# Kernel optimization log

Measured on AMD Instinct MI355X. Metric: run time of the kernel, lower is better.

Reference implementation:

```python
import jax, jax.numpy as jnp
import numpy as np

B, N, C, S, K = 2, 2048, 64, 128, 8
RADIUS_PX = 1.5
RAD_POW = 2
TAU = 1.0  # accumulation_tau
RADIUS_NDC = RADIUS_PX / S * 2.0  # radius converted to NDC units, as in forward


def setup_inputs() -> dict:
    key = jax.random.key(0)
    k1, k2, k3 = jax.random.split(key, 3)
    xy = jax.random.uniform(k1, (B, N, 2), minval=-1.0, maxval=1.0)
    z = jax.random.uniform(k2, (B, N, 1), minval=0.1, maxval=5.0)
    pts3D = jnp.concatenate([xy, z], axis=-1)  # [B,N,3] NDC points, z>0
    src = jax.random.normal(k3, (B, C, N), dtype=jnp.float32)  # [B,C,N] features
    return {"pts3D": pts3D, "src": src}


def _rasterize_composite(pts3D, src):
    # sign flip of x,y as in forward (pts3D[:,:,0]=-..., pts3D[:,:,1]=-...)
    pts = pts3D * jnp.array([-1.0, -1.0, 1.0], dtype=pts3D.dtype)
    x, y, z = pts[..., 0], pts[..., 1], pts[..., 2]  # each [B,N]
    # NDC pixel centers (pytorch3d convention: +1 at index 0)
    pix = 1.0 - (2.0 * jnp.arange(S, dtype=pts.dtype) + 1.0) / S  # [S]
    dx2 = (pix[None, :, None] - x[:, None, :]) ** 2  # [B,S_x,N]
    dy2 = (pix[None, :, None] - y[:, None, :]) ** 2  # [B,S_y,N]
    dist2 = dy2[:, :, None, :] + dx2[:, None, :, :]  # [B,S,S,N] squared NDC dist
    in_rad = (dist2 < RADIUS_NDC ** 2) & (z[:, None, None, :] > 0)
    zbuf = jnp.where(in_rad, z[:, None, None, :], jnp.inf)
    # per-pixel z-buffer: K points with smallest z among in-radius points
    negz, idx = jax.lax.top_k(-zbuf, K)  # [B,S,S,K]
    valid = (negz > -jnp.inf).astype(pts.dtype)
    dist_sel = jnp.take_along_axis(dist2, idx, axis=-1)  # [B,S,S,K]
    # dist = dist / radius**rad_pow ; alphas = (1 - clamp(dist,1e-3,1)**0.5)**tau
    dist_n = dist_sel / (RADIUS_NDC ** RAD_POW)
    alphas = (1.0 - jnp.sqrt(jnp.clip(dist_n, 0.001, 1.0))) ** TAU
    alphas = alphas * valid  # empty z-buffer slots contribute nothing
    # gather point features: [B,S,S,K,C]
    feats = src.transpose(0, 2, 1)  # [B,N,C]
    g = jnp.take_along_axis(feats, idx.reshape(B, -1)[..., None], axis=1)
    g = g.reshape(B, S, S, K, C)
    # front-to-back alpha compositing: w_k = a_k * prod_{j<k}(1-a_j)
    trans = jnp.cumprod(1.0 - alphas, axis=-1)
    T = jnp.concatenate([jnp.ones_like(alphas[..., :1]), trans[..., :-1]], axis=-1)
    w = alphas * T  # [B,S,S,K]
    return jnp.einsum('byxk,byxkc->bcyx', w, g)  # [B,C,S,S]


def reference(pts3D, src):
    return _rasterize_composite(pts3D, src)
```

## Files before the change

kernel.cpp:

```cpp
#include <hip/hip_runtime.h>
#include <math.h>

#define NN 2048
#define CC 64
#define SS 128
#define KK 8
#define TCAP 128

#define R2f    0.00054931640625f
#define RNDCf  0.0234375f

__global__ __launch_bounds__(256) void raster_fused_kernel(
    const float* __restrict__ pts3D,
    const float* __restrict__ src,
    float* __restrict__ out)
{
    __shared__ float scx[TCAP];
    __shared__ float scy[TCAP];
    __shared__ unsigned long long skey[TCAP];
    __shared__ int scount;
    __shared__ float sW[KK * 64];
    __shared__ int   sI[KK * 64];

    const int tid = threadIdx.x;
    const int blk = blockIdx.x;
    const int b   = blk >> 8;
    const int tb  = blk & 255;
    const int Y0  = (tb >> 2) * 2;
    const int X0  = (tb & 3) * 32;

    if (tid == 0) scount = 0;
    __syncthreads();

    const float cxmax = 1.0f - (2.0f * (float)X0 + 1.0f) / (float)SS;
    const float cxmin = 1.0f - (2.0f * (float)(X0 + 31) + 1.0f) / (float)SS;
    const float cymax = 1.0f - (2.0f * (float)Y0 + 1.0f) / (float)SS;
    const float cymin = 1.0f - (2.0f * (float)(Y0 + 1) + 1.0f) / (float)SS;
    const float Rm = RNDCf + 1e-6f;

    const float* P = pts3D + (size_t)b * NN * 3;
#pragma unroll
    for (int j = 0; j < NN / 256; ++j) {
        int n = tid + j * 256;
        const float* p = P + (size_t)n * 3;
        float x = -p[0], y = -p[1], z = p[2];
        if (z > 0.0f &&
            x >= cxmin - Rm && x <= cxmax + Rm &&
            y >= cymin - Rm && y <= cymax + Rm) {
            int slot = atomicAdd(&scount, 1);
            if (slot < TCAP) {
                scx[slot] = x;
                scy[slot] = y;
                skey[slot] = ((unsigned long long)__float_as_uint(z) << 32) | (unsigned)n;
            }
        }
    }
    __syncthreads();
    const int cn = min(scount, TCAP);

    if (tid < 64) {
        const int col = tid & 31, r = tid >> 5;
        const int ix = X0 + col, iy = Y0 + r;
        const float pcx = 1.0f - (2.0f * (float)ix + 1.0f) / (float)SS;
        const float pcy = 1.0f - (2.0f * (float)iy + 1.0f) / (float)SS;

        const unsigned long long SENT = ~0ULL;
        unsigned long long s[KK];
        float sd[KK];
#pragma unroll
        for (int j = 0; j < KK; ++j) { s[j] = SENT; sd[j] = 0.0f; }

        for (int i = 0; i < cn; ++i) {
            float dx = pcx - scx[i];
            float dy = pcy - scy[i];
            float d2 = dy * dy + dx * dx;
            unsigned long long k = skey[i];
            if (d2 < R2f && k < s[KK - 1]) {
                float dd = d2;
#pragma unroll
                for (int j = 0; j < KK; ++j) {
                    if (k < s[j]) {
                        unsigned long long tk = s[j]; s[j] = k; k = tk;
                        float td = sd[j]; sd[j] = dd; dd = td;
                    }
                }
            }
        }

        float T = 1.0f;
#pragma unroll
        for (int k = 0; k < KK; ++k) {
            float w = 0.0f; int id = 0;
            if (s[k] != SENT) {
                id = (int)(unsigned)(s[k] & 0xffffffffu);
                float dn = sd[k] / R2f;
                dn = fminf(fmaxf(dn, 0.001f), 1.0f);
                float a = 1.0f - sqrtf(dn);
                w = a * T;
                T *= (1.0f - a);
            }
            sW[k * 64 + tid] = w;
            sI[k * 64 + tid] = id;
        }
    }
    __syncthreads();

    const int px = tid & 63;
    const int cg = tid >> 6;
    float w[KK]; int id[KK];
#pragma unroll
    for (int k = 0; k < KK; ++k) {
        w[k]  = sW[k * 64 + px];
        id[k] = sI[k * 64 + px];
    }
    const int col = px & 31, r = px >> 5;
    float* O = out + (size_t)b * CC * (SS * SS) + (size_t)(Y0 + r) * SS + (X0 + col);
    const float* F = src + (size_t)b * CC * NN;
#pragma unroll 4
    for (int cc = 0; cc < CC / 4; ++cc) {
        int c = cg * (CC / 4) + cc;
        const float* Fc = F + (size_t)c * NN;
        float acc = 0.0f;
#pragma unroll
        for (int k = 0; k < KK; ++k) acc += w[k] * Fc[id[k]];
        O[(size_t)c * (SS * SS)] = acc;
    }
}

extern "C" void kernel_launch(void* const* d_in, const int* in_sizes, int n_in,
                              void* d_out, int out_size, void* d_ws, size_t ws_size,
                              hipStream_t stream) {
    const float* pts3D = (const float*)d_in[0];
    const float* src   = (const float*)d_in[1];
    float* out = (float*)d_out;
    (void)in_sizes; (void)n_in; (void)out_size; (void)d_ws; (void)ws_size;

    raster_fused_kernel<<<dim3(512), dim3(256), 0, stream>>>(pts3D, src, out);
}
```

Baseline: 73.95 us.

## Pre-sort candidates by depth and split channels across twice as many blocks

Candidate points for each tile are now rank-sorted by (z, index) key in shared memory. Each pixel thread then takes the first K in-radius points in that order, which replaces the per-pixel insertion sort over K registers. The grid doubles: each tile is processed by two blocks that each write half of the channels. The launch-bounds occupancy hint is raised as well. The cost is that point culling and the sort run twice per tile, plus an O(cn^2) rank computation in shared memory.

```diff
diff --git a/kernel.cpp b/kernel.cpp
--- a/kernel.cpp
+++ b/kernel.cpp
@@ -10,26 +10,29 @@
 #define R2f    0.00054931640625f
 #define RNDCf  0.0234375f
 
-__global__ __launch_bounds__(256) void raster_fused_kernel(
+__global__ __launch_bounds__(256, 4) void raster_fused_kernel(
     const float* __restrict__ pts3D,
     const float* __restrict__ src,
     float* __restrict__ out)
 {
-    __shared__ float scx[TCAP];
-    __shared__ float scy[TCAP];
+    __shared__ float scx[TCAP], scy[TCAP];
     __shared__ unsigned long long skey[TCAP];
-    __shared__ int scount;
+    __shared__ float ssx[TCAP], ssy[TCAP];
+    __shared__ int   sid[TCAP];
+    __shared__ int   scount;
     __shared__ float sW[KK * 64];
     __shared__ int   sI[KK * 64];
 
-    const int tid = threadIdx.x;
-    const int blk = blockIdx.x;
-    const int b   = blk >> 8;
-    const int tb  = blk & 255;
-    const int Y0  = (tb >> 2) * 2;
-    const int X0  = (tb & 3) * 32;
+    const int tid  = threadIdx.x;
+    const int blk  = blockIdx.x;
+    const int half = blk & 1;
+    const int X0   = ((blk >> 1) & 3) * 32;
+    const int Y0   = ((blk >> 3) & 63) * 2;
+    const int b    = blk >> 9;
 
     if (tid == 0) scount = 0;
+    sW[tid] = 0.0f; sW[tid + 256] = 0.0f;
+    sI[tid] = 0;    sI[tid + 256] = 0;
     __syncthreads();
 
     const float cxmax = 1.0f - (2.0f * (float)X0 + 1.0f) / (float)SS;
@@ -42,8 +45,7 @@
 #pragma unroll
     for (int j = 0; j < NN / 256; ++j) {
         int n = tid + j * 256;
-        const float* p = P + (size_t)n * 3;
-        float x = -p[0], y = -p[1], z = p[2];
+        float x = -P[n * 3 + 0], y = -P[n * 3 + 1], z = P[n * 3 + 2];
         if (z > 0.0f &&
             x >= cxmin - Rm && x <= cxmax + Rm &&
             y >= cymin - Rm && y <= cymax + Rm) {
@@ -58,49 +60,36 @@
     __syncthreads();
     const int cn = min(scount, TCAP);
 
+    if (tid < cn) {
+        unsigned long long mykey = skey[tid];
+        int rank = 0;
+        for (int j = 0; j < cn; ++j)
+            rank += (skey[j] < mykey) ? 1 : 0;
+        ssx[rank] = scx[tid];
+        ssy[rank] = scy[tid];
+        sid[rank] = (int)(unsigned)(mykey & 0xffffffffu);
+    }
+    __syncthreads();
+
     if (tid < 64) {
         const int col = tid & 31, r = tid >> 5;
-        const int ix = X0 + col, iy = Y0 + r;
-        const float pcx = 1.0f - (2.0f * (float)ix + 1.0f) / (float)SS;
-        const float pcy = 1.0f - (2.0f * (float)iy + 1.0f) / (float)SS;
-
-        const unsigned long long SENT = ~0ULL;
-        unsigned long long s[KK];
-        float sd[KK];
-#pragma unroll
-        for (int j = 0; j < KK; ++j) { s[j] = SENT; sd[j] = 0.0f; }
-
+        const float pcx = 1.0f - (2.0f * (float)(X0 + col) + 1.0f) / (float)SS;
+        const float pcy = 1.0f - (2.0f * (float)(Y0 + r) + 1.0f) / (float)SS;
+        float T = 1.0f;
+        int cnt = 0;
         for (int i = 0; i < cn; ++i) {
-            float dx = pcx - scx[i];
-            float dy = pcy - scy[i];
+            float dx = pcx - ssx[i];
+            float dy = pcy - ssy[i];
             float d2 = dy * dy + dx * dx;
-            unsigned long long k = skey[i];
-            if (d2 < R2f && k < s[KK - 1]) {
-                float dd = d2;
-#pragma unroll
-                for (int j = 0; j < KK; ++j) {
-                    if (k < s[j]) {
-                        unsigned long long tk = s[j]; s[j] = k; k = tk;
-                        float td = sd[j]; sd[j] = dd; dd = td;
-                    }
-                }
-            }
-        }
-
-        float T = 1.0f;
-#pragma unroll
-        for (int k = 0; k < KK; ++k) {
-            float w = 0.0f; int id = 0;
-            if (s[k] != SENT) {
-                id = (int)(unsigned)(s[k] & 0xffffffffu);
-                float dn = sd[k] / R2f;
+            if (d2 < R2f && cnt < KK) {
+                float dn = d2 / R2f;
                 dn = fminf(fmaxf(dn, 0.001f), 1.0f);
                 float a = 1.0f - sqrtf(dn);
-                w = a * T;
+                sW[cnt * 64 + tid] = a * T;
+                sI[cnt * 64 + tid] = sid[i];
                 T *= (1.0f - a);
+                ++cnt;
             }
-            sW[k * 64 + tid] = w;
-            sI[k * 64 + tid] = id;
         }
     }
     __syncthreads();
@@ -116,9 +105,9 @@
     const int col = px & 31, r = px >> 5;
     float* O = out + (size_t)b * CC * (SS * SS) + (size_t)(Y0 + r) * SS + (X0 + col);
     const float* F = src + (size_t)b * CC * NN;
-#pragma unroll 4
-    for (int cc = 0; cc < CC / 4; ++cc) {
-        int c = cg * (CC / 4) + cc;
+#pragma unroll
+    for (int cc = 0; cc < 8; ++cc) {
+        int c = half * 32 + cg * 8 + cc;
         const float* Fc = F + (size_t)c * NN;
         float acc = 0.0f;
 #pragma unroll
@@ -135,5 +124,5 @@
     float* out = (float*)d_out;
     (void)in_sizes; (void)n_in; (void)out_size; (void)d_ws; (void)ws_size;
 
-    raster_fused_kernel<<<dim3(512), dim3(256), 0, stream>>>(pts3D, src, out);
+    raster_fused_kernel<<<dim3(1024), dim3(256), 0, stream>>>(pts3D, src, out);
 }
```

Measured after the change: 71.94 us. 1.03x faster.
